# Performance work log

Measured on AMD Instinct MI355X. Metric: run time of the kernel, lower is better.

## Reference

```python
import jax, jax.numpy as jnp
import numpy as np
import math

D = 1024  # output_dim (power of 2)
IN = 1024  # input dim
CAP = int(math.log2(D))  # number of butterfly stages


def _gen_indices(s):
    """Static FFT-butterfly index lists (numpy, computed at trace time)."""
    def ind_s(k):
        if k == 0:
            return [np.array([1, 0])]
        temp = np.arange(2 ** k)
        list0 = [np.concatenate([temp + 2 ** k, temp])]
        list1 = ind_s(k - 1)
        for i in range(k):
            list0.append(np.concatenate([list1[i], list1[i] + 2 ** k]))
        return list0

    t = ind_s(int(math.log2(s // 2)))
    cap = int(math.log2(s))
    ind_exe = [np.asarray(t[i], dtype=np.int32) for i in range(cap)]
    ind_param = []
    for i in range(cap):
        ind = np.concatenate([np.arange(0, s, 2 ** i) + j for j in range(2 ** i)]).astype(np.int32)
        ind_param.append(ind)
    return ind_exe, ind_param


IND_EXE, IND_PARAM = _gen_indices(D)


def setup_inputs() -> dict:
    key = jax.random.key(0)
    ks = jax.random.split(key, 9)
    B = 8192
    x = jax.random.normal(ks[0], (B, IN), dtype=jnp.float32)
    state = jax.random.normal(ks[1], (B, D), dtype=jnp.float32)
    theta = jax.random.uniform(ks[2], (CAP, D // 2), minval=-3.14, maxval=3.14, dtype=jnp.float32)
    U = jax.random.uniform(ks[3], (IN, 3 * D), minval=-0.01, maxval=0.01, dtype=jnp.float32)
    W_r = jax.random.uniform(ks[4], (D, D), minval=-0.01, maxval=0.01, dtype=jnp.float32)
    W_g = jax.random.uniform(ks[5], (D, D), minval=-0.01, maxval=0.01, dtype=jnp.float32)
    bias_r = jnp.full((D,), 2.0, dtype=jnp.float32)
    bias_g = jnp.zeros((D,), dtype=jnp.float32)
    bias_c = jnp.full((D,), 0.01, dtype=jnp.float32)
    return {"x": x, "state": state, "theta": theta, "U": U, "W_r": W_r,
            "W_g": W_g, "bias_r": bias_r, "bias_g": bias_g, "bias_c": bias_c}


def reference(x, state, theta, U, W_r, W_g, bias_r, bias_g, bias_c):
    # fft_param: rotation coefficients, permuted by the static ind_param lists
    cos_list = jnp.concatenate([jnp.cos(theta), jnp.cos(theta)], axis=1)   # [CAP, D]
    sin_list = jnp.concatenate([jnp.sin(theta), -jnp.sin(theta)], axis=1)  # [CAP, D]
    v1 = jnp.stack([cos_list[i][IND_PARAM[i]] for i in range(CAP)])  # [CAP, D]
    v2 = jnp.stack([sin_list[i][IND_PARAM[i]] for i in range(CAP)])  # [CAP, D]

    Ux = x @ U                                   # [B, 3D]
    U_cx, U_rx, U_gx = jnp.split(Ux, 3, axis=1)  # each [B, D]
    r = jax.nn.sigmoid(U_rx + state @ W_r + bias_r)
    g = jax.nn.sigmoid(U_gx + state @ W_g + bias_g)

    # butterfly orthogonal rotation of the state
    h = state
    for i in range(CAP):
        h = h * v1[i] + (h * v2[i])[:, IND_EXE[i]]

    # modReLU
    pre = r * h + U_cx
    c = jnp.sign(pre) * jax.nn.relu(jnp.abs(pre) + 0.001 + bias_c)

    out = g * state + (1.0 - g) * c
    return out
```

## Files before the change

### kernel.cpp

```cpp
#include <hip/hip_runtime.h>
#include <hip/hip_bf16.h>
#include <stdint.h>


typedef __bf16 bf16x8 __attribute__((ext_vector_type(8)));
typedef __bf16 bf16x4 __attribute__((ext_vector_type(4)));
typedef __bf16 bf16x2 __attribute__((ext_vector_type(2)));
typedef float f32x4 __attribute__((ext_vector_type(4)));

#define B_ROWS 8192

__device__ __forceinline__ void async16(__bf16* lds, const __hip_bfloat16* g) {
    __builtin_amdgcn_global_load_lds((const __attribute__((address_space(1))) void*)g,
                                     (__attribute__((address_space(3))) void*)lds,
                                     16, 0, 0);
}

__global__ __launch_bounds__(256) void prep_all(const float* __restrict__ x,
                                                const float* __restrict__ state,
                                                const float* __restrict__ theta,
                                                const float* __restrict__ U,
                                                const float* __restrict__ Wr,
                                                const float* __restrict__ Wg,
                                                __hip_bfloat16* __restrict__ xs,
                                                __hip_bfloat16* __restrict__ Wt0,
                                                __hip_bfloat16* __restrict__ Wt12,
                                                float* __restrict__ v1,
                                                float* __restrict__ v2) {
    __shared__ float tile[32][33];
    const int id = blockIdx.x;
    if (id < 8192) {
        const int row = id;
        const int col = threadIdx.x * 8;
        const float* src = (col < 1024) ? (x + (size_t)row * 1024 + col)
                                        : (state + (size_t)row * 1024 + (col - 1024));
        float4 a = *(const float4*)src;
        float4 b = *(const float4*)(src + 4);
        bf16x8 v;
        v[0] = (__bf16)a.x; v[1] = (__bf16)a.y; v[2] = (__bf16)a.z; v[3] = (__bf16)a.w;
        v[4] = (__bf16)b.x; v[5] = (__bf16)b.y; v[6] = (__bf16)b.z; v[7] = (__bf16)b.w;
        *(bf16x8*)((__bf16*)xs + (size_t)row * 2048 + col) = v;
    } else if (id < 13312) {
        const int wid = id - 8192;
        const float* src; int srcN, scol, sk;
        __hip_bfloat16* dst; int dstStride, dn, dk;
        if (wid < 1024) {
            int nx = wid & 31, ky = wid >> 5;
            src = U; srcN = 3072; scol = nx * 32; sk = ky * 32;
            dst = Wt0; dstStride = 1024; dn = nx * 32; dk = ky * 32;
        } else {
            int id2 = wid - 1024;
            int nx = id2 & 63, ky = id2 >> 6;
            int n0 = nx * 32, k0 = ky * 32;
            dst = Wt12; dstStride = 2048; dn = n0; dk = k0;
            if (k0 < 1024)      { src = U;  srcN = 3072; scol = 1024 + n0; sk = k0; }
            else if (n0 < 1024) { src = Wr; srcN = 1024; scol = n0;        sk = k0 - 1024; }
            else                { src = Wg; srcN = 1024; scol = n0 - 1024; sk = k0 - 1024; }
        }
        const int tx = threadIdx.x & 31, ty = threadIdx.x >> 5;
#pragma unroll
        for (int s = 0; s < 4; ++s)
            tile[ty + s * 8][tx] = src[(size_t)(sk + ty + s * 8) * srcN + scol + tx];
        __syncthreads();
#pragma unroll
        for (int s = 0; s < 4; ++s)
            dst[(size_t)(dn + ty + s * 8) * dstStride + dk + tx] = __float2bfloat16(tile[tx][ty + s * 8]);
    } else {
        int idx = (id - 13312) * 256 + threadIdx.x;
        int i = idx >> 10;
        int j = idx & 1023;
        int Q = 1024 >> i;
        int j0 = j / Q;
        int m = j & (Q - 1);
        int q = (m << i) + j0;
        float th = theta[i * 512 + (q & 511)];
        float c = cosf(th);
        float s = sinf(th);
        v1[idx] = c;
        v2[idx] = (q < 512) ? s : -s;
    }
}

__global__ __launch_bounds__(512, 4) void gemm_fused(const __hip_bfloat16* __restrict__ xs,
                                                     const __hip_bfloat16* __restrict__ Wt0,
                                                     const __hip_bfloat16* __restrict__ Wt12,
                                                     const float* __restrict__ bias_r,
                                                     const float* __restrict__ bias_g,
                                                     __hip_bfloat16* __restrict__ P) {
    __shared__ __align__(16) __bf16 As[128 * 32];
    __shared__ __align__(16) __bf16 Bs1[128 * 32];
    __shared__ __align__(16) __bf16 Bs2[128 * 32];

    const int nt = blockIdx.x;
    const int mt = blockIdx.y;
    const int mBase = mt * 128;

    const int t = threadIdx.x;
    const int lane = t & 63;
    const int wv = t >> 6;
    const int wm = wv & 1;
    const int wn = wv >> 1;
    const int r0 = lane & 15;
    const int gq = lane >> 4;

    const int srow = t >> 2;
    const int sjj = ((t & 3) ^ ((srow >> 1) & 3)) * 8;

    const __hip_bfloat16* A = xs + (size_t)mBase * 2048;

    if (nt < 8) {
        const int c0 = nt * 128;
        const __hip_bfloat16* B1 = Wt12 + (size_t)c0 * 2048;
        const __hip_bfloat16* B2 = Wt12 + (size_t)(1024 + c0) * 2048;

        f32x4 accr[4][2], accg[4][2];
        const f32x4 zero = {0.f, 0.f, 0.f, 0.f};
#pragma unroll
        for (int i = 0; i < 4; ++i)
#pragma unroll
            for (int j = 0; j < 2; ++j) { accr[i][j] = zero; accg[i][j] = zero; }

        for (int k0 = 0; k0 < 2048; k0 += 32) {
            size_t off = (size_t)srow * 2048 + k0 + sjj;
            async16(&As[t * 8], A + off);
            async16(&Bs1[t * 8], B1 + off);
            async16(&Bs2[t * 8], B2 + off);
            __syncthreads();

            bf16x8 af[4], b1[2], b2[2];
#pragma unroll
            for (int i = 0; i < 4; ++i) {
                int row = wm * 64 + i * 16 + r0;
                int cc = row * 4 + (gq ^ ((row >> 1) & 3));
                af[i] = *reinterpret_cast<const bf16x8*>(&As[cc * 8]);
            }
#pragma unroll
            for (int j = 0; j < 2; ++j) {
                int row = wn * 32 + j * 16 + r0;
                int cc = row * 4 + (gq ^ ((row >> 1) & 3));
                b1[j] = *reinterpret_cast<const bf16x8*>(&Bs1[cc * 8]);
                b2[j] = *reinterpret_cast<const bf16x8*>(&Bs2[cc * 8]);
            }
#pragma unroll
            for (int i = 0; i < 4; ++i)
#pragma unroll
                for (int j = 0; j < 2; ++j) {
                    accr[i][j] = __builtin_amdgcn_mfma_f32_16x16x32_bf16(af[i], b1[j], accr[i][j], 0, 0, 0);
                    accg[i][j] = __builtin_amdgcn_mfma_f32_16x16x32_bf16(af[i], b2[j], accg[i][j], 0, 0, 0);
                }
            __syncthreads();
        }

#pragma unroll
        for (int i = 0; i < 4; ++i) {
#pragma unroll
            for (int j = 0; j < 2; ++j) {
#pragma unroll
                for (int reg = 0; reg < 4; ++reg) {
                    int row = mBase + wm * 64 + i * 16 + gq * 4 + reg;
                    int c = c0 + wn * 32 + j * 16 + r0;
                    float zr = 1.0f / (1.0f + __expf(-(accr[i][j][reg] + bias_r[c])));
                    float zg = 1.0f / (1.0f + __expf(-(accg[i][j][reg] + bias_g[c])));
                    bf16x2 pk;
                    pk[0] = (__bf16)zr;
                    pk[1] = (__bf16)zg;
                    *(bf16x2*)((__bf16*)P + (size_t)row * 3072 + 1024 + 2 * c) = pk;
                }
            }
        }
    } else {
        const int c0 = (nt - 8) * 128;
        const __hip_bfloat16* Bb = Wt0 + (size_t)c0 * 1024;

        f32x4 acc[4][2];
        const f32x4 zero = {0.f, 0.f, 0.f, 0.f};
#pragma unroll
        for (int i = 0; i < 4; ++i)
#pragma unroll
            for (int j = 0; j < 2; ++j) acc[i][j] = zero;

        for (int k0 = 0; k0 < 1024; k0 += 32) {
            async16(&As[t * 8], A + (size_t)srow * 2048 + k0 + sjj);
            async16(&Bs1[t * 8], Bb + (size_t)srow * 1024 + k0 + sjj);
            __syncthreads();

            bf16x8 af[4], bf[2];
#pragma unroll
            for (int i = 0; i < 4; ++i) {
                int row = wm * 64 + i * 16 + r0;
                int cc = row * 4 + (gq ^ ((row >> 1) & 3));
                af[i] = *reinterpret_cast<const bf16x8*>(&As[cc * 8]);
            }
#pragma unroll
            for (int j = 0; j < 2; ++j) {
                int row = wn * 32 + j * 16 + r0;
                int cc = row * 4 + (gq ^ ((row >> 1) & 3));
                bf[j] = *reinterpret_cast<const bf16x8*>(&Bs1[cc * 8]);
            }
#pragma unroll
            for (int i = 0; i < 4; ++i)
#pragma unroll
                for (int j = 0; j < 2; ++j)
                    acc[i][j] = __builtin_amdgcn_mfma_f32_16x16x32_bf16(af[i], bf[j], acc[i][j], 0, 0, 0);
            __syncthreads();
        }

#pragma unroll
        for (int i = 0; i < 4; ++i) {
#pragma unroll
            for (int j = 0; j < 2; ++j) {
#pragma unroll
                for (int reg = 0; reg < 4; ++reg) {
                    int row = mBase + wm * 64 + i * 16 + gq * 4 + reg;
                    int c = c0 + wn * 32 + j * 16 + r0;
                    P[(size_t)row * 3072 + c] = __float2bfloat16(acc[i][j][reg]);
                }
            }
        }
    }
}

__global__ __launch_bounds__(256) void fuse_kernel(const float* __restrict__ state,
                                                   const __hip_bfloat16* __restrict__ P,
                                                   const float* __restrict__ v1,
                                                   const float* __restrict__ v2,
                                                   const float* __restrict__ bias_c,
                                                   float* __restrict__ out) {
    __shared__ float hbuf[8][1024];
    const int t = threadIdx.x;
    const int rowBase = blockIdx.x * 8;

    float h[8][4];
    float sv[8][4];
#pragma unroll
    for (int r = 0; r < 8; ++r) {
        float4 s4 = ((const float4*)(state + (size_t)(rowBase + r) * 1024))[t];
        h[r][0] = s4.x; h[r][1] = s4.y; h[r][2] = s4.z; h[r][3] = s4.w;
        sv[r][0] = s4.x; sv[r][1] = s4.y; sv[r][2] = s4.z; sv[r][3] = s4.w;
        *(float4*)&hbuf[r][4 * t] = s4;
    }

    {
        __syncthreads();
        float4 w1 = *(const float4*)&v1[4 * t];
        float4 w2 = *(const float4*)&v2[4 * (t ^ 128)];
        const float w1v[4] = {w1.x, w1.y, w1.z, w1.w};
        const float w2v[4] = {w2.x, w2.y, w2.z, w2.w};
#pragma unroll
        for (int r = 0; r < 8; ++r) {
            float4 pr = *(const float4*)&hbuf[r][4 * (t ^ 128)];
            const float pv[4] = {pr.x, pr.y, pr.z, pr.w};
#pragma unroll
            for (int e = 0; e < 4; ++e) h[r][e] = h[r][e] * w1v[e] + pv[e] * w2v[e];
        }
        __syncthreads();
    }
    {
#pragma unroll
        for (int r = 0; r < 8; ++r)
            *(float4*)&hbuf[r][4 * t] = (float4){h[r][0], h[r][1], h[r][2], h[r][3]};
        __syncthreads();
        float4 w1 = *(const float4*)&v1[1024 + 4 * t];
        float4 w2 = *(const float4*)&v2[1024 + 4 * (t ^ 64)];
        const float w1v[4] = {w1.x, w1.y, w1.z, w1.w};
        const float w2v[4] = {w2.x, w2.y, w2.z, w2.w};
#pragma unroll
        for (int r = 0; r < 8; ++r) {
            float4 pr = *(const float4*)&hbuf[r][4 * (t ^ 64)];
            const float pv[4] = {pr.x, pr.y, pr.z, pr.w};
#pragma unroll
            for (int e = 0; e < 4; ++e) h[r][e] = h[r][e] * w1v[e] + pv[e] * w2v[e];
        }
    }
#pragma unroll
    for (int i = 2; i <= 7; ++i) {
        const int H = 512 >> i;
        const int lm = H >> 2;
        float4 w1 = *(const float4*)&v1[i * 1024 + 4 * t];
        float4 w2 = *(const float4*)&v2[i * 1024 + 4 * (t ^ lm)];
        const float w1v[4] = {w1.x, w1.y, w1.z, w1.w};
        const float w2v[4] = {w2.x, w2.y, w2.z, w2.w};
#pragma unroll
        for (int r = 0; r < 8; ++r) {
#pragma unroll
            for (int e = 0; e < 4; ++e) {
                float p = __shfl_xor(h[r][e], lm, 64);
                h[r][e] = h[r][e] * w1v[e] + p * w2v[e];
            }
        }
    }
    {
        float4 w1 = *(const float4*)&v1[8 * 1024 + 4 * t];
        float4 w2 = *(const float4*)&v2[8 * 1024 + 4 * t];
        const float w1v[4] = {w1.x, w1.y, w1.z, w1.w};
        const float w2v[4] = {w2.x, w2.y, w2.z, w2.w};
#pragma unroll
        for (int r = 0; r < 8; ++r) {
            float nh[4];
#pragma unroll
            for (int e = 0; e < 4; ++e) nh[e] = h[r][e] * w1v[e] + h[r][e ^ 2] * w2v[e ^ 2];
#pragma unroll
            for (int e = 0; e < 4; ++e) h[r][e] = nh[e];
        }
        float4 u1 = *(const float4*)&v1[9 * 1024 + 4 * t];
        float4 u2 = *(const float4*)&v2[9 * 1024 + 4 * t];
        const float u1v[4] = {u1.x, u1.y, u1.z, u1.w};
        const float u2v[4] = {u2.x, u2.y, u2.z, u2.w};
#pragma unroll
        for (int r = 0; r < 8; ++r) {
            float nh[4];
#pragma unroll
            for (int e = 0; e < 4; ++e) nh[e] = h[r][e] * u1v[e] + h[r][e ^ 1] * u2v[e ^ 1];
#pragma unroll
            for (int e = 0; e < 4; ++e) h[r][e] = nh[e];
        }
    }

    const float4 bc = ((const float4*)bias_c)[t];
    const float bcv[4] = {bc.x, bc.y, bc.z, bc.w};
#pragma unroll
    for (int r = 0; r < 8; ++r) {
        const int row = rowBase + r;
        const __hip_bfloat16* Pr = P + (size_t)row * 3072;
        bf16x4 ux = *(const bf16x4*)((const __bf16*)Pr + 4 * t);
        bf16x8 rg = *(const bf16x8*)((const __bf16*)Pr + 1024 + 8 * t);
        float o[4];
#pragma unroll
        for (int e = 0; e < 4; ++e) {
            float Ucx = (float)ux[e];
            float rr  = (float)rg[2 * e];
            float gg  = (float)rg[2 * e + 1];
            float pre = rr * h[r][e] + Ucx;
            float mag = fabsf(pre) + 0.001f + bcv[e];
            float c = (pre > 0.f) ? mag : ((pre < 0.f) ? -mag : 0.f);
            o[e] = gg * sv[r][e] + (1.f - gg) * c;
        }
        ((float4*)(out + (size_t)row * 1024))[t] = (float4){o[0], o[1], o[2], o[3]};
    }
}

extern "C" void kernel_launch(void* const* d_in, const int* in_sizes, int n_in,
                              void* d_out, int out_size, void* d_ws, size_t ws_size,
                              hipStream_t stream) {
    const float* x      = (const float*)d_in[0];
    const float* state  = (const float*)d_in[1];
    const float* theta  = (const float*)d_in[2];
    const float* U      = (const float*)d_in[3];
    const float* W_r    = (const float*)d_in[4];
    const float* W_g    = (const float*)d_in[5];
    const float* bias_r = (const float*)d_in[6];
    const float* bias_g = (const float*)d_in[7];
    const float* bias_c = (const float*)d_in[8];
    float* out = (float*)d_out;

    __hip_bfloat16* xs   = (__hip_bfloat16*)d_ws;
    __hip_bfloat16* Wt0  = xs + (size_t)B_ROWS * 2048;
    __hip_bfloat16* Wt12 = Wt0 + (size_t)1024 * 1024;
    __hip_bfloat16* P    = Wt12 + (size_t)2048 * 2048;
    float* v1 = (float*)(P + (size_t)B_ROWS * 3072);
    float* v2 = v1 + 10 * 1024;

    prep_all<<<13352, 256, 0, stream>>>(x, state, theta, U, W_r, W_g, xs, Wt0, Wt12, v1, v2);
    gemm_fused<<<dim3(16, 64), 512, 0, stream>>>(xs, Wt0, Wt12, bias_r, bias_g, P);
    fuse_kernel<<<1024, 256, 0, stream>>>(state, P, v1, v2, bias_c, out);
}
```

Before: 282.4 us.

## Restructure gate GEMM into 256x256 double-buffered tiles with interleaved r/g weights

Rewrites the fused GEMM so each block computes a 256-row tile. It first runs the r/g gate GEMM over K=2048 with 256 interleaved output columns, then reuses the block for the U_c GEMM over K=1024. The prep kernel interleaves the W_r and W_g rows so one B tile covers both gates. The main loop uses double-buffered LDS with K=64 stages, explicit waitcnt and barrier scheduling, s_setprio around the MFMA bursts, and an L2-friendly swizzle of block indices. This aims to raise arithmetic intensity and overlap loads with MFMAs, at the cost of much more LDS and registers (occupancy bound 2) and a fragile hand-scheduled pipeline.

```diff
diff --git a/kernel.cpp b/kernel.cpp
--- a/kernel.cpp
+++ b/kernel.cpp
@@ -44,15 +44,18 @@
         const int wid = id - 8192;
         const float* src; int srcN, scol, sk;
         __hip_bfloat16* dst; int dstStride, dn, dk;
+        bool ilv;
         if (wid < 1024) {
             int nx = wid & 31, ky = wid >> 5;
             src = U; srcN = 3072; scol = nx * 32; sk = ky * 32;
             dst = Wt0; dstStride = 1024; dn = nx * 32; dk = ky * 32;
+            ilv = false;
         } else {
             int id2 = wid - 1024;
             int nx = id2 & 63, ky = id2 >> 6;
             int n0 = nx * 32, k0 = ky * 32;
             dst = Wt12; dstStride = 2048; dn = n0; dk = k0;
+            ilv = true;
             if (k0 < 1024)      { src = U;  srcN = 3072; scol = 1024 + n0; sk = k0; }
             else if (n0 < 1024) { src = Wr; srcN = 1024; scol = n0;        sk = k0 - 1024; }
             else                { src = Wg; srcN = 1024; scol = n0 - 1024; sk = k0 - 1024; }
@@ -63,8 +66,11 @@
             tile[ty + s * 8][tx] = src[(size_t)(sk + ty + s * 8) * srcN + scol + tx];
         __syncthreads();
 #pragma unroll
-        for (int s = 0; s < 4; ++s)
-            dst[(size_t)(dn + ty + s * 8) * dstStride + dk + tx] = __float2bfloat16(tile[tx][ty + s * 8]);
+        for (int s = 0; s < 4; ++s) {
+            int n = dn + ty + s * 8;
+            int wrow = ilv ? ((n < 1024) ? 2 * n : 2 * (n - 1024) + 1) : n;
+            dst[(size_t)wrow * dstStride + dk + tx] = __float2bfloat16(tile[tx][ty + s * 8]);
+        }
     } else {
         int idx = (id - 13312) * 256 + threadIdx.x;
         int i = idx >> 10;
@@ -81,19 +87,25 @@
     }
 }
 
-__global__ __launch_bounds__(512, 4) void gemm_fused(const __hip_bfloat16* __restrict__ xs,
+#define BAR()   asm volatile("s_barrier" ::: "memory")
+#define LGKM0() asm volatile("s_waitcnt lgkmcnt(0)" ::: "memory")
+#define LGKM8() asm volatile("s_waitcnt lgkmcnt(8)" ::: "memory")
+#define VMCNT(n) asm volatile("s_waitcnt vmcnt(" #n ")" ::: "memory")
+
+__global__ __launch_bounds__(512, 2) void gemm_fused(const __hip_bfloat16* __restrict__ xs,
                                                      const __hip_bfloat16* __restrict__ Wt0,
                                                      const __hip_bfloat16* __restrict__ Wt12,
                                                      const float* __restrict__ bias_r,
                                                      const float* __restrict__ bias_g,
                                                      __hip_bfloat16* __restrict__ P) {
-    __shared__ __align__(16) __bf16 As[128 * 32];
-    __shared__ __align__(16) __bf16 Bs1[128 * 32];
-    __shared__ __align__(16) __bf16 Bs2[128 * 32];
-
-    const int nt = blockIdx.x;
-    const int mt = blockIdx.y;
-    const int mBase = mt * 128;
+    __shared__ __align__(16) __bf16 As[2][16384];
+    __shared__ __align__(16) __bf16 Bs[2][16384];
+
+    const int bid = blockIdx.x;
+    const int swz = (bid & 7) * 32 + (bid >> 3);
+    const int nt = swz & 7;
+    const int mt = swz >> 3;
+    const int mBase = mt * 256;
 
     const int t = threadIdx.x;
     const int lane = t & 63;
@@ -103,122 +115,198 @@
     const int r0 = lane & 15;
     const int gq = lane >> 4;
 
-    const int srow = t >> 2;
-    const int sjj = ((t & 3) ^ ((srow >> 1) & 3)) * 8;
-
-    const __hip_bfloat16* A = xs + (size_t)mBase * 2048;
-
-    if (nt < 8) {
-        const int c0 = nt * 128;
-        const __hip_bfloat16* B1 = Wt12 + (size_t)c0 * 2048;
-        const __hip_bfloat16* B2 = Wt12 + (size_t)(1024 + c0) * 2048;
-
-        f32x4 accr[4][2], accg[4][2];
-        const f32x4 zero = {0.f, 0.f, 0.f, 0.f};
-#pragma unroll
-        for (int i = 0; i < 4; ++i)
-#pragma unroll
-            for (int j = 0; j < 2; ++j) { accr[i][j] = zero; accg[i][j] = zero; }
-
-        for (int k0 = 0; k0 < 2048; k0 += 32) {
-            size_t off = (size_t)srow * 2048 + k0 + sjj;
-            async16(&As[t * 8], A + off);
-            async16(&Bs1[t * 8], B1 + off);
-            async16(&Bs2[t * 8], B2 + off);
-            __syncthreads();
-
-            bf16x8 af[4], b1[2], b2[2];
-#pragma unroll
-            for (int i = 0; i < 4; ++i) {
-                int row = wm * 64 + i * 16 + r0;
-                int cc = row * 4 + (gq ^ ((row >> 1) & 3));
-                af[i] = *reinterpret_cast<const bf16x8*>(&As[cc * 8]);
+    const int coff0 = ((gq ^ (r0 & 7)) << 3);
+    const int coff1 = coff0 ^ 32;
+    const int rowA = wm * 128 + r0;
+    const int rowB = wn * 64 + r0;
+    const int rowBu = wn * 32 + r0;
+
+    const int s_row = t >> 3;
+    const int s_q8 = (((t & 7) ^ (s_row & 7)) << 3);
+
+    const __hip_bfloat16* Ag = xs + (size_t)(mBase + s_row) * 2048 + s_q8;
+    const __hip_bfloat16* Bg = Wt12 + (size_t)(nt * 256 + s_row) * 2048 + s_q8;
+    const __hip_bfloat16* Cg = Wt0 + (size_t)(nt * 128 + s_row) * 1024 + s_q8;
+
+#define STG_A(buf, h, kt) do { \
+    async16(&As[buf][(((h) << 10) + t) << 3],       Ag + (size_t)((h) * 128) * 2048 + (kt) * 64); \
+    async16(&As[buf][(((h) << 10) + 512 + t) << 3], Ag + (size_t)((h) * 128 + 64) * 2048 + (kt) * 64); \
+} while (0)
+#define STG_B(buf, h, kt) do { \
+    async16(&Bs[buf][(((h) << 10) + t) << 3],       Bg + (size_t)((h) * 128) * 2048 + (kt) * 64); \
+    async16(&Bs[buf][(((h) << 10) + 512 + t) << 3], Bg + (size_t)((h) * 128 + 64) * 2048 + (kt) * 64); \
+} while (0)
+#define STG_C(buf, kt) do { \
+    async16(&Bs[buf][t << 3],         Cg + (kt) * 64); \
+    async16(&Bs[buf][(512 + t) << 3], Cg + (size_t)64 * 1024 + (kt) * 64); \
+} while (0)
+
+#define LOAD_AFL(bufArr) do { _Pragma("unroll") for (int i = 0; i < 4; ++i) { \
+    afl[i][0] = *(const bf16x8*)&bufArr[(rowA + i * 16) * 64 + coff0]; \
+    afl[i][1] = *(const bf16x8*)&bufArr[(rowA + i * 16) * 64 + coff1]; } } while (0)
+#define LOAD_AFH(bufArr) do { _Pragma("unroll") for (int i = 0; i < 4; ++i) { \
+    afh[i][0] = *(const bf16x8*)&bufArr[(rowA + 64 + i * 16) * 64 + coff0]; \
+    afh[i][1] = *(const bf16x8*)&bufArr[(rowA + 64 + i * 16) * 64 + coff1]; } } while (0)
+#define LOAD_BB(bufArr, base) do { _Pragma("unroll") for (int j = 0; j < 2; ++j) { \
+    bb[j][0] = *(const bf16x8*)&bufArr[((base) + j * 16) * 64 + coff0]; \
+    bb[j][1] = *(const bf16x8*)&bufArr[((base) + j * 16) * 64 + coff1]; } } while (0)
+#define MFMA8(I0, J0, af) do { _Pragma("unroll") for (int i = 0; i < 4; ++i) \
+    _Pragma("unroll") for (int j = 0; j < 2; ++j) { \
+    acc[(I0) + i][(J0) + j] = __builtin_amdgcn_mfma_f32_16x16x32_bf16(af[i][0], bb[j][0], acc[(I0) + i][(J0) + j], 0, 0, 0); \
+    acc[(I0) + i][(J0) + j] = __builtin_amdgcn_mfma_f32_16x16x32_bf16(af[i][1], bb[j][1], acc[(I0) + i][(J0) + j], 0, 0, 0); } } while (0)
+
+    f32x4 acc[8][4];
+    bf16x8 afl[4][2], afh[4][2], bb[2][2];
+    const f32x4 zero = {0.f, 0.f, 0.f, 0.f};
+#pragma unroll
+    for (int i = 0; i < 8; ++i)
+#pragma unroll
+        for (int j = 0; j < 4; ++j) acc[i][j] = zero;
+
+    STG_A(0, 0, 0); STG_A(0, 1, 0);
+    STG_B(0, 0, 0); STG_B(0, 1, 0);
+    STG_A(1, 0, 1); STG_A(1, 1, 1);
+    VMCNT(4);
+    BAR();
+
+#pragma unroll 1
+    for (int u = 0; u < 16; ++u) {
+        const int kt1 = 2 * u + 1;
+        const int kt2 = (2 * u + 2) & 31;
+        const int kt3 = (2 * u + 3) & 31;
+
+        LOAD_AFL(As[0]);
+        LOAD_BB(Bs[0], rowB);
+        STG_B(1, 0, kt1);
+        LGKM8();
+        BAR(); LGKM0();
+        __builtin_amdgcn_s_setprio(1); MFMA8(0, 0, afl); __builtin_amdgcn_s_setprio(0);
+        BAR();
+        LOAD_AFH(As[0]);
+        STG_B(1, 1, kt1);
+        BAR(); LGKM0();
+        __builtin_amdgcn_s_setprio(1); MFMA8(4, 0, afh); __builtin_amdgcn_s_setprio(0);
+        BAR();
+        LOAD_BB(Bs[0], rowB + 32);
+        STG_A(0, 0, kt2);
+        BAR(); LGKM0();
+        __builtin_amdgcn_s_setprio(1); MFMA8(0, 2, afl); __builtin_amdgcn_s_setprio(0);
+        BAR();
+        STG_A(0, 1, kt2);
+        BAR();
+        __builtin_amdgcn_s_setprio(1); MFMA8(4, 2, afh); __builtin_amdgcn_s_setprio(0);
+        VMCNT(4);
+        BAR();
+        LOAD_AFL(As[1]);
+        LOAD_BB(Bs[1], rowB);
+        STG_B(0, 0, kt2);
+        LGKM8();
+        BAR(); LGKM0();
+        __builtin_amdgcn_s_setprio(1); MFMA8(0, 0, afl); __builtin_amdgcn_s_setprio(0);
+        BAR();
+        LOAD_AFH(As[1]);
+        STG_B(0, 1, kt2);
+        BAR(); LGKM0();
+        __builtin_amdgcn_s_setprio(1); MFMA8(4, 0, afh); __builtin_amdgcn_s_setprio(0);
+        BAR();
+        LOAD_BB(Bs[1], rowB + 32);
+        STG_A(1, 0, kt3);
+        BAR(); LGKM0();
+        __builtin_amdgcn_s_setprio(1); MFMA8(0, 2, afl); __builtin_amdgcn_s_setprio(0);
+        BAR();
+        STG_A(1, 1, kt3);
+        BAR();
+        __builtin_amdgcn_s_setprio(1); MFMA8(4, 2, afh); __builtin_amdgcn_s_setprio(0);
+        VMCNT(4);
+        BAR();
+    }
+
+    VMCNT(0);
+    BAR();
+
+    STG_A(0, 0, 0); STG_A(0, 1, 0);
+    STG_C(0, 0);
+    STG_C(1, 1);
+
+#pragma unroll
+    for (int j = 0; j < 4; ++j) {
+        const int ct = nt * 256 + wn * 64 + j * 16 + r0;
+        const float bias = (r0 & 1) ? bias_g[ct >> 1] : bias_r[ct >> 1];
+#pragma unroll
+        for (int i = 0; i < 8; ++i) {
+#pragma unroll
+            for (int reg = 0; reg < 4; ++reg) {
+                const int row = mBase + wm * 128 + i * 16 + gq * 4 + reg;
+                const float z = 1.0f / (1.0f + __expf(-(acc[i][j][reg] + bias)));
+                P[(size_t)row * 3072 + 1024 + ct] = __float2bfloat16(z);
             }
-#pragma unroll
-            for (int j = 0; j < 2; ++j) {
-                int row = wn * 32 + j * 16 + r0;
-                int cc = row * 4 + (gq ^ ((row >> 1) & 3));
-                b1[j] = *reinterpret_cast<const bf16x8*>(&Bs1[cc * 8]);
-                b2[j] = *reinterpret_cast<const bf16x8*>(&Bs2[cc * 8]);
+        }
+    }
+
+    VMCNT(0);
+    BAR();
+
+#pragma unroll
+    for (int i = 0; i < 8; ++i)
+#pragma unroll
+        for (int j = 0; j < 2; ++j) acc[i][j] = zero;
+
+#pragma unroll 1
+    for (int u = 0; u < 8; ++u) {
+        const int kt1 = 2 * u + 1;
+        const int kt2 = (2 * u + 2) & 15;
+        const int kt3 = (2 * u + 3) & 15;
+
+        LOAD_AFL(As[0]);
+        LOAD_BB(Bs[0], rowBu);
+        STG_A(1, 0, kt1); STG_A(1, 1, kt1);
+        LGKM8();
+        BAR(); LGKM0();
+        __builtin_amdgcn_s_setprio(1); MFMA8(0, 0, afl); __builtin_amdgcn_s_setprio(0);
+        BAR();
+        LOAD_AFH(As[0]);
+        STG_C(0, kt2);
+        BAR(); LGKM0();
+        __builtin_amdgcn_s_setprio(1); MFMA8(4, 0, afh); __builtin_amdgcn_s_setprio(0);
+        VMCNT(2);
+        BAR();
+        LOAD_AFL(As[1]);
+        LOAD_BB(Bs[1], rowBu);
+        STG_A(0, 0, kt2); STG_A(0, 1, kt2);
+        LGKM8();
+        BAR(); LGKM0();
+        __builtin_amdgcn_s_setprio(1); MFMA8(0, 0, afl); __builtin_amdgcn_s_setprio(0);
+        BAR();
+        LOAD_AFH(As[1]);
+        STG_C(1, kt3);
+        BAR(); LGKM0();
+        __builtin_amdgcn_s_setprio(1); MFMA8(4, 0, afh); __builtin_amdgcn_s_setprio(0);
+        VMCNT(2);
+        BAR();
+    }
+
+#pragma unroll
+    for (int j = 0; j < 2; ++j) {
+        const int col = nt * 128 + wn * 32 + j * 16 + r0;
+#pragma unroll
+        for (int i = 0; i < 8; ++i) {
+#pragma unroll
+            for (int reg = 0; reg < 4; ++reg) {
+                const int row = mBase + wm * 128 + i * 16 + gq * 4 + reg;
+                P[(size_t)row * 3072 + col] = __float2bfloat16(acc[i][j][reg]);
             }
-#pragma unroll
-            for (int i = 0; i < 4; ++i)
-#pragma unroll
-                for (int j = 0; j < 2; ++j) {
-                    accr[i][j] = __builtin_amdgcn_mfma_f32_16x16x32_bf16(af[i], b1[j], accr[i][j], 0, 0, 0);
-                    accg[i][j] = __builtin_amdgcn_mfma_f32_16x16x32_bf16(af[i], b2[j], accg[i][j], 0, 0, 0);
-                }
-            __syncthreads();
-        }
-
-#pragma unroll
-        for (int i = 0; i < 4; ++i) {
-#pragma unroll
-            for (int j = 0; j < 2; ++j) {
-#pragma unroll
-                for (int reg = 0; reg < 4; ++reg) {
-                    int row = mBase + wm * 64 + i * 16 + gq * 4 + reg;
-                    int c = c0 + wn * 32 + j * 16 + r0;
-                    float zr = 1.0f / (1.0f + __expf(-(accr[i][j][reg] + bias_r[c])));
-                    float zg = 1.0f / (1.0f + __expf(-(accg[i][j][reg] + bias_g[c])));
-                    bf16x2 pk;
-                    pk[0] = (__bf16)zr;
-                    pk[1] = (__bf16)zg;
-                    *(bf16x2*)((__bf16*)P + (size_t)row * 3072 + 1024 + 2 * c) = pk;
-                }
-            }
-        }
-    } else {
-        const int c0 = (nt - 8) * 128;
-        const __hip_bfloat16* Bb = Wt0 + (size_t)c0 * 1024;
-
-        f32x4 acc[4][2];
-        const f32x4 zero = {0.f, 0.f, 0.f, 0.f};
-#pragma unroll
-        for (int i = 0; i < 4; ++i)
-#pragma unroll
-            for (int j = 0; j < 2; ++j) acc[i][j] = zero;
-
-        for (int k0 = 0; k0 < 1024; k0 += 32) {
-            async16(&As[t * 8], A + (size_t)srow * 2048 + k0 + sjj);
-            async16(&Bs1[t * 8], Bb + (size_t)srow * 1024 + k0 + sjj);
-            __syncthreads();
-
-            bf16x8 af[4], bf[2];
-#pragma unroll
-            for (int i = 0; i < 4; ++i) {
-                int row = wm * 64 + i * 16 + r0;
-                int cc = row * 4 + (gq ^ ((row >> 1) & 3));
-                af[i] = *reinterpret_cast<const bf16x8*>(&As[cc * 8]);
-            }
-#pragma unroll
-            for (int j = 0; j < 2; ++j) {
-                int row = wn * 32 + j * 16 + r0;
-                int cc = row * 4 + (gq ^ ((row >> 1) & 3));
-                bf[j] = *reinterpret_cast<const bf16x8*>(&Bs1[cc * 8]);
-            }
-#pragma unroll
-            for (int i = 0; i < 4; ++i)
-#pragma unroll
-                for (int j = 0; j < 2; ++j)
-                    acc[i][j] = __builtin_amdgcn_mfma_f32_16x16x32_bf16(af[i], bf[j], acc[i][j], 0, 0, 0);
-            __syncthreads();
-        }
-
-#pragma unroll
-        for (int i = 0; i < 4; ++i) {
-#pragma unroll
-            for (int j = 0; j < 2; ++j) {
-#pragma unroll
-                for (int reg = 0; reg < 4; ++reg) {
-                    int row = mBase + wm * 64 + i * 16 + gq * 4 + reg;
-                    int c = c0 + wn * 32 + j * 16 + r0;
-                    P[(size_t)row * 3072 + c] = __float2bfloat16(acc[i][j][reg]);
-                }
-            }
-        }
-    }
+        }
+    }
+    VMCNT(0);
 }
+
+#undef STG_A
+#undef STG_B
+#undef STG_C
+#undef LOAD_AFL
+#undef LOAD_AFH
+#undef LOAD_BB
+#undef MFMA8
 
 __global__ __launch_bounds__(256) void fuse_kernel(const float* __restrict__ state,
                                                    const __hip_bfloat16* __restrict__ P,
@@ -361,6 +449,6 @@
     float* v2 = v1 + 10 * 1024;
 
     prep_all<<<13352, 256, 0, stream>>>(x, state, theta, U, W_r, W_g, xs, Wt0, Wt12, v1, v2);
-    gemm_fused<<<dim3(16, 64), 512, 0, stream>>>(xs, Wt0, Wt12, bias_r, bias_g, P);
+    gemm_fused<<<256, 512, 0, stream>>>(xs, Wt0, Wt12, bias_r, bias_g, P);
     fuse_kernel<<<1024, 256, 0, stream>>>(state, P, v1, v2, bias_c, out);
 }
```

Measured after the change: 242.9 us. 1.16x faster.
